# Kernel optimization log

Measured on AMD Instinct MI355X. Metric: run time of the kernel, lower is better.

The kernel has to match this reference:

```python
import jax, jax.numpy as jnp
import numpy as np
import math

B, N, L = 1, 256, 384
DM, DP, H, D = 256, 128, 8, 32  # d_msa, d_pair, n_head, d_hidden


def ln(x, g, b):
    m = x.mean(-1, keepdims=True)
    v = ((x - m) ** 2).mean(-1, keepdims=True)
    return (x - m) * jax.lax.rsqrt(v + 1e-5) * g + b


def setup_inputs() -> dict:
    key = jax.random.key(0)
    ks = jax.random.split(key, 12)
    s = 0.02
    return dict(
        msa=jax.random.normal(ks[0], (B, N, L, DM), jnp.float32),
        pair=jax.random.normal(ks[1], (B, L, L, DP), jnp.float32),
        ln_msa_g=jnp.ones((DM,), jnp.float32),
        ln_msa_b=jnp.zeros((DM,), jnp.float32),
        ln_pair_g=jnp.ones((DP,), jnp.float32),
        ln_pair_b=jnp.zeros((DP,), jnp.float32),
        sw_wq=s * jax.random.normal(ks[2], (DM, H * D), jnp.float32),
        sw_bq=jnp.zeros((H * D,), jnp.float32),
        sw_wk=s * jax.random.normal(ks[3], (DM, H * D), jnp.float32),
        sw_bk=jnp.zeros((H * D,), jnp.float32),
        wq=s * jax.random.normal(ks[4], (DM, H * D), jnp.float32),
        wk=s * jax.random.normal(ks[5], (DM, H * D), jnp.float32),
        wv=s * jax.random.normal(ks[6], (DM, H * D), jnp.float32),
        wb=s * jax.random.normal(ks[7], (DP, H), jnp.float32),
        wg=s * jax.random.normal(ks[8], (DM, H * D), jnp.float32),
        bg=jnp.ones((H * D,), jnp.float32),
        wo=s * jax.random.normal(ks[9], (H * D, DM), jnp.float32),
        bo=jnp.zeros((DM,), jnp.float32),
    )


def reference(msa, pair, ln_msa_g, ln_msa_b, ln_pair_g, ln_pair_b,
              sw_wq, sw_bq, sw_wk, sw_bk, wq, wk, wv, wb, wg, bg, wo, bo):
    m = ln(msa, ln_msa_g, ln_msa_b)  # (B,N,L,DM) -- LayerNorm(msa)
    inv_sqrt_d = 1.0 / math.sqrt(D)

    # --- SequenceWeight: attention of target seq (row 0) over all MSA rows ---
    qsw = ((m[:, 0] @ sw_wq) + sw_bq).reshape(B, 1, L, H, D) * inv_sqrt_d
    ksw = ((m @ sw_wk) + sw_bk).reshape(B, N, L, H, D)
    sw_logits = jnp.einsum('bqihd,bnihd->bnihq', qsw, ksw)  # (B,N,L,H,1)
    seq_weight = jax.nn.softmax(sw_logits, axis=1)  # softmax over MSA depth N; dropout is eval no-op

    # --- row attention with pair bias ---
    q = (m @ wq).reshape(B, N, L, H, D) * seq_weight  # query scaled by per-row seq weight
    k = (m @ wk).reshape(B, N, L, H, D) * inv_sqrt_d
    attn = jnp.einsum('bnihd,bnjhd->bijh', q, k)  # sum over MSA rows n -> (B,L,L,H)
    attn = attn + ln(pair, ln_pair_g, ln_pair_b) @ wb  # additive pair bias
    attn = jax.nn.softmax(attn, axis=-2)  # softmax over j (dim=-2)

    v = (m @ wv).reshape(B, N, L, H, D)
    out = jnp.einsum('bijh,bnjhd->bnihd', attn, v).reshape(B, N, L, H * D)
    gate = jax.nn.sigmoid((m @ wg) + bg)
    out = out * gate
    return out @ wo + bo  # (B,N,L,DM)
```

## Files before the change

kernel.cpp:

```cpp
#include <hip/hip_runtime.h>
#include <math.h>

typedef unsigned short u16;
typedef __bf16 bf16x8 __attribute__((ext_vector_type(8)));
typedef float f32x4 __attribute__((ext_vector_type(4)));

#define DEV static __device__ __forceinline__

DEV float b2f(u16 u) { union { unsigned int i; float f; } v; v.i = ((unsigned int)u) << 16; return v.f; }
DEV u16 f2b(float f) {
  union { float f; unsigned int i; } v; v.f = f;
  unsigned int x = v.i;
  unsigned int r = (x + 0x7fffu + ((x >> 16) & 1u)) >> 16;
  return (u16)r;
}
DEV bf16x8 load8bf(const u16* p) {
  union { uint4 u; bf16x8 b; } t;
  t.u = *(const uint4*)p;
  return t.b;
}
DEV float wave_sum(float x) {
  for (int m = 32; m >= 1; m >>= 1) x += __shfl_xor(x, m, 64);
  return x;
}
DEV float wave_max(float x) {
  for (int m = 32; m >= 1; m >>= 1) x = fmaxf(x, __shfl_xor(x, m, 64));
  return x;
}

__global__ __launch_bounds__(256) void detect_dtype(const u16* __restrict__ probe, int* __restrict__ flag) {
  __shared__ float red[4];
  int wave = threadIdx.x >> 6, lane = threadIdx.x & 63;
  float v = fabsf(b2f(probe[threadIdx.x]));
  v = wave_max(v);
  if (lane == 0) red[wave] = v;
  __syncthreads();
  if (threadIdx.x == 0) {
    float m = fmaxf(fmaxf(red[0], red[1]), fmaxf(red[2], red[3]));
    *flag = (m > 1e10f) ? 1 : 0;
  }
}

struct SmallCvt {
  const void* src[9];
  int n[9];
  int off[9];
};
__global__ __launch_bounds__(256) void cvt_small(SmallCvt s, u16* __restrict__ dst, const int* __restrict__ flagp) {
  int isf32 = *flagp;
  int a = blockIdx.x;
  const void* sp = s.src[a];
  for (int i = threadIdx.x; i < s.n[a]; i += 256) {
    float v = isf32 ? ((const float*)sp)[i] : b2f(((const u16*)sp)[i]);
    dst[s.off[a] + i] = f2b(v);
  }
}

__global__ __launch_bounds__(256) void ln_msa_k(const void* __restrict__ xv, const u16* __restrict__ g,
                                                const u16* __restrict__ b, u16* __restrict__ out,
                                                const int* __restrict__ flagp) {
  int isf32 = *flagp;
  int wave = threadIdx.x >> 6, lane = threadIdx.x & 63;
  size_t row = (size_t)blockIdx.x * 4 + wave;
  float f0, f1, f2, f3;
  if (isf32) {
    float4 v = *(const float4*)((const float*)xv + row * 256 + lane * 4);
    f0 = v.x; f1 = v.y; f2 = v.z; f3 = v.w;
  } else {
    ushort4 v = *(const ushort4*)((const u16*)xv + row * 256 + lane * 4);
    f0 = b2f(v.x); f1 = b2f(v.y); f2 = b2f(v.z); f3 = b2f(v.w);
  }
  float s = wave_sum(f0 + f1 + f2 + f3);
  float s2 = wave_sum(f0 * f0 + f1 * f1 + f2 * f2 + f3 * f3);
  float mean = s * (1.f / 256.f);
  float inv = rsqrtf(s2 * (1.f / 256.f) - mean * mean + 1e-5f);
  int c0 = lane * 4;
  ushort4 gv = *(const ushort4*)(g + c0);
  ushort4 bv = *(const ushort4*)(b + c0);
  ushort4 o;
  o.x = f2b((f0 - mean) * inv * b2f(gv.x) + b2f(bv.x));
  o.y = f2b((f1 - mean) * inv * b2f(gv.y) + b2f(bv.y));
  o.z = f2b((f2 - mean) * inv * b2f(gv.z) + b2f(bv.z));
  o.w = f2b((f3 - mean) * inv * b2f(gv.w) + b2f(bv.w));
  *(ushort4*)(out + row * 256 + c0) = o;
}

struct TransArgs {
  const void* src[7];
  u16* dst[7];
};
__global__ __launch_bounds__(256) void transpose_w(TransArgs t, const int* __restrict__ flagp) {
  __shared__ float tile[32][33];
  int isf32 = *flagp;
  int m = blockIdx.z;
  const void* s = t.src[m];
  u16* d = t.dst[m];
  int bx = blockIdx.x * 32, by = blockIdx.y * 32;
  int c = threadIdx.x & 31, r0 = threadIdx.x >> 5;
  for (int rr = r0; rr < 32; rr += 8) {
    int idx = (by + rr) * 256 + bx + c;
    tile[rr][c] = isf32 ? ((const float*)s)[idx] : b2f(((const u16*)s)[idx]);
  }
  __syncthreads();
  for (int rr = r0; rr < 32; rr += 8) d[(bx + rr) * 256 + by + c] = f2b(tile[c][rr]);
}

__global__ __launch_bounds__(256) void gemmA(const u16* __restrict__ A, size_t aoff,
                                             const u16* __restrict__ WT, const u16* __restrict__ bias,
                                             void* __restrict__ outv, size_t ooff, int mode, float alpha,
                                             const float* __restrict__ sw, int n0sw,
                                             const int* __restrict__ flagp, int out_flag,
                                             const u16* __restrict__ WT2, void* __restrict__ out2,
                                             int mode_b, float alpha_b) {
  int isf32 = *flagp;
  int n0;
  if (WT2) {
    if (blockIdx.y >> 1) { WT = WT2; outv = out2; mode = mode_b; alpha = alpha_b; bias = nullptr; }
    n0 = (blockIdx.y & 1) * 128;
  } else {
    n0 = blockIdx.y * 128;
  }
  int i0 = blockIdx.x * 128;
  int wave = threadIdx.x >> 6, lane = threadIdx.x & 63;
  int wr = wave >> 1, wc = wave & 1;
  int l15 = lane & 15, quad = lane >> 4;
  const f32x4 fz = {0.f, 0.f, 0.f, 0.f};
  f32x4 acc[4][4];
  for (int mi = 0; mi < 4; ++mi)
    for (int ni = 0; ni < 4; ++ni) acc[mi][ni] = fz;
  int arow = i0 + wr * 64 + l15;
  int brow = n0 + wc * 64 + l15;
  const u16* ap = A + (aoff + (size_t)arow) * 256 + quad * 8;
  const u16* bp = WT + (size_t)brow * 256 + quad * 8;
  for (int k0 = 0; k0 < 256; k0 += 32) {
    bf16x8 a[4], b[4];
#pragma unroll
    for (int mi = 0; mi < 4; ++mi) a[mi] = load8bf(ap + mi * 16 * 256 + k0);
#pragma unroll
    for (int ni = 0; ni < 4; ++ni) b[ni] = load8bf(bp + ni * 16 * 256 + k0);
#pragma unroll
    for (int mi = 0; mi < 4; ++mi)
#pragma unroll
      for (int ni = 0; ni < 4; ++ni)
        acc[mi][ni] = __builtin_amdgcn_mfma_f32_16x16x32_bf16(a[mi], b[ni], acc[mi][ni], 0, 0, 0);
  }
  int f32out = out_flag && isf32;
  int nloc = blockIdx.x / 3;
  if (mode == 3) {
#pragma unroll
    for (int mi = 0; mi < 4; ++mi) {
      int ib = i0 + wr * 64 + mi * 16 + quad * 4 - nloc * 384;
#pragma unroll
      for (int ni = 0; ni < 4; ++ni) {
        int col = n0 + wc * 64 + ni * 16 + l15;
        ushort4 o;
        o.x = f2b(acc[mi][ni][0]);
        o.y = f2b(acc[mi][ni][1]);
        o.z = f2b(acc[mi][ni][2]);
        o.w = f2b(acc[mi][ni][3]);
        *(ushort4*)((u16*)outv + ((size_t)(nloc * 256 + col)) * 384 + ib) = o;
      }
    }
    return;
  }
#pragma unroll
  for (int mi = 0; mi < 4; ++mi) {
    int rbase = i0 + wr * 64 + mi * 16 + quad * 4;
#pragma unroll
    for (int ni = 0; ni < 4; ++ni) {
      int col = n0 + wc * 64 + ni * 16 + l15;
      float bv = bias ? b2f(bias[col]) : 0.f;
#pragma unroll
      for (int r = 0; r < 4; ++r) {
        float val = (acc[mi][ni][r] + bv) * alpha;
        if (mode == 2) {
          int i = rbase - nloc * 384 + r;
          int h = col >> 5;
          val *= sw[((size_t)(i * 8 + h)) * 256 + (n0sw + nloc)];
        }
        size_t idx = (ooff + (size_t)(rbase + r)) * 256 + col;
        if (mode == 1) {
          float gate = 1.f / (1.f + expf(-val));
          ((u16*)outv)[idx] = f2b(b2f(((u16*)outv)[idx]) * gate);
        } else if (f32out) {
          ((float*)outv)[idx] = val;
        } else {
          ((u16*)outv)[idx] = f2b(val);
        }
      }
    }
  }
}

__global__ __launch_bounds__(256) void sw_logits_c(const u16* __restrict__ qsw, const u16* __restrict__ kswc,
                                                   float* __restrict__ swlog, int n0) {
  int nl = blockIdx.y;
  int t = blockIdx.x * 256 + threadIdx.x;
  int i = t >> 3, h = t & 7;
  const u16* kr = kswc + ((size_t)(nl * 384 + i)) * 256 + h * 32;
  const u16* qr = qsw + (size_t)i * 256 + h * 32;
  float dot = 0.f;
#pragma unroll
  for (int d8 = 0; d8 < 4; ++d8) {
    union { uint4 u; u16 us[8]; } ku, qu;
    ku.u = *(const uint4*)(kr + d8 * 8);
    qu.u = *(const uint4*)(qr + d8 * 8);
#pragma unroll
    for (int j = 0; j < 8; ++j) dot += b2f(ku.us[j]) * b2f(qu.us[j]);
  }
  swlog[(size_t)(i * 8 + h) * 256 + n0 + nl] = dot;
}

__global__ __launch_bounds__(256) void sw_softmax(float* __restrict__ swlog) {
  __shared__ float red[4];
  float* p = swlog + (size_t)blockIdx.x * 256;
  int wave = threadIdx.x >> 6, lane = threadIdx.x & 63;
  float x = p[threadIdx.x];
  float m = wave_max(x);
  if (lane == 0) red[wave] = m;
  __syncthreads();
  float mx = fmaxf(fmaxf(red[0], red[1]), fmaxf(red[2], red[3]));
  __syncthreads();
  float e = expf(x - mx);
  float s = wave_sum(e);
  if (lane == 0) red[wave] = s;
  __syncthreads();
  float sum = red[0] + red[1] + red[2] + red[3];
  p[threadIdx.x] = e / sum;
}

__global__ __launch_bounds__(256) void pair_bias(const void* __restrict__ pairv, const u16* __restrict__ g,
                                                 const u16* __restrict__ b, const u16* __restrict__ wb,
                                                 float* __restrict__ attn, const int* __restrict__ flagp) {
  int isf32 = *flagp;
  int wave = threadIdx.x >> 6, lane = threadIdx.x & 63;
  size_t row = (size_t)blockIdx.x * 4 + wave;
  float v0, v1;
  if (isf32) {
    const float* pf = (const float*)pairv + row * 128 + lane * 2;
    v0 = pf[0]; v1 = pf[1];
  } else {
    const u16* pr = (const u16*)pairv + row * 128 + lane * 2;
    v0 = b2f(pr[0]); v1 = b2f(pr[1]);
  }
  float s = wave_sum(v0 + v1);
  float s2 = wave_sum(v0 * v0 + v1 * v1);
  float mean = s * (1.f / 128.f);
  float var = s2 * (1.f / 128.f) - mean * mean;
  float inv = rsqrtf(var + 1e-5f);
  int c0 = lane * 2;
  v0 = (v0 - mean) * inv * b2f(g[c0]) + b2f(b[c0]);
  v1 = (v1 - mean) * inv * b2f(g[c0 + 1]) + b2f(b[c0 + 1]);
  float ph[8];
  const u16* w0 = wb + c0 * 8;
#pragma unroll
  for (int h = 0; h < 8; ++h) ph[h] = v0 * b2f(w0[h]) + v1 * b2f(w0[8 + h]);
#pragma unroll
  for (int m = 32; m >= 1; m >>= 1)
#pragma unroll
    for (int h = 0; h < 8; ++h) ph[h] += __shfl_xor(ph[h], m, 64);
  if (lane == 0) {
#pragma unroll
    for (int h = 0; h < 8; ++h) attn[(size_t)h * 147456 + row] = ph[h];
  }
}

__global__ __launch_bounds__(256) void qk_accum_c(const u16* __restrict__ qc, const u16* __restrict__ kc,
                                                  float* __restrict__ attn, int nlen) {
  int h = blockIdx.y;
  int i0 = (blockIdx.x % 3) * 128, j0 = (blockIdx.x / 3) * 128;
  int nb = blockIdx.z * nlen;
  int wave = threadIdx.x >> 6, lane = threadIdx.x & 63;
  int wr = wave >> 1, wc = wave & 1;
  int l15 = lane & 15, quad = lane >> 4;
  const f32x4 fz = {0.f, 0.f, 0.f, 0.f};
  f32x4 acc[4][4];
  for (int mi = 0; mi < 4; ++mi)
    for (int ni = 0; ni < 4; ++ni) acc[mi][ni] = fz;
  int arow = i0 + wr * 64 + l15;
  int brow = j0 + wc * 64 + l15;
  for (int n = nb; n < nb + nlen; ++n) {
    size_t base = (size_t)n * 384;
    const u16* ap = qc + (base + arow) * 256 + h * 32 + quad * 8;
    const u16* bp = kc + (base + brow) * 256 + h * 32 + quad * 8;
    bf16x8 a[4], b[4];
#pragma unroll
    for (int mi = 0; mi < 4; ++mi) a[mi] = load8bf(ap + mi * 16 * 256);
#pragma unroll
    for (int ni = 0; ni < 4; ++ni) b[ni] = load8bf(bp + ni * 16 * 256);
#pragma unroll
    for (int mi = 0; mi < 4; ++mi)
#pragma unroll
      for (int ni = 0; ni < 4; ++ni)
        acc[mi][ni] = __builtin_amdgcn_mfma_f32_16x16x32_bf16(a[mi], b[ni], acc[mi][ni], 0, 0, 0);
  }
#pragma unroll
  for (int mi = 0; mi < 4; ++mi)
#pragma unroll
    for (int ni = 0; ni < 4; ++ni) {
      int i = i0 + wr * 64 + mi * 16 + quad * 4;
      int j = j0 + wc * 64 + ni * 16 + l15;
#pragma unroll
      for (int r = 0; r < 4; ++r)
        atomicAdd(&attn[(size_t)h * 147456 + (size_t)(i + r) * 384 + j], acc[mi][ni][r]);
    }
}

__global__ __launch_bounds__(384) void attn_softmax_k(const float* __restrict__ attn, u16* __restrict__ attn_bf) {
  __shared__ float red[6];
  size_t r = blockIdx.x;
  const float* p = attn + r * 384;
  int wave = threadIdx.x >> 6, lane = threadIdx.x & 63;
  float x = p[threadIdx.x];
  float m = wave_max(x);
  if (lane == 0) red[wave] = m;
  __syncthreads();
  float mx = red[0];
#pragma unroll
  for (int i = 1; i < 6; ++i) mx = fmaxf(mx, red[i]);
  __syncthreads();
  float e = expf(x - mx);
  float s = wave_sum(e);
  if (lane == 0) red[wave] = s;
  __syncthreads();
  float sum = 0.f;
#pragma unroll
  for (int i = 0; i < 6; ++i) sum += red[i];
  attn_bf[r * 384 + threadIdx.x] = f2b(e / sum);
}

__global__ __launch_bounds__(256) void pv_gemm(const u16* __restrict__ attn_bf, const u16* __restrict__ vt,
                                               u16* __restrict__ oc) {
  int h = blockIdx.z;
  int i0 = blockIdx.x * 128;
  int c0 = blockIdx.y * 128;
  int wave = threadIdx.x >> 6, lane = threadIdx.x & 63;
  int wr = wave >> 1, wc = wave & 1;
  int l15 = lane & 15, quad = lane >> 4;
  const f32x4 fz = {0.f, 0.f, 0.f, 0.f};
  f32x4 acc[4][4];
  for (int mi = 0; mi < 4; ++mi)
    for (int ni = 0; ni < 4; ++ni) acc[mi][ni] = fz;
  int arow = i0 + wr * 64 + l15;
  const u16* ap = attn_bf + ((size_t)(h * 384 + arow)) * 384 + quad * 8;
  const u16* bp[4];
#pragma unroll
  for (int ni = 0; ni < 4; ++ni) {
    int col = c0 + wc * 64 + ni * 16 + l15;
    bp[ni] = vt + ((size_t)((col >> 5) * 256 + h * 32 + (col & 31))) * 384 + quad * 8;
  }
  for (int k0 = 0; k0 < 384; k0 += 32) {
    bf16x8 a[4], b[4];
#pragma unroll
    for (int mi = 0; mi < 4; ++mi) a[mi] = load8bf(ap + mi * 16 * 384 + k0);
#pragma unroll
    for (int ni = 0; ni < 4; ++ni) b[ni] = load8bf(bp[ni] + k0);
#pragma unroll
    for (int mi = 0; mi < 4; ++mi)
#pragma unroll
      for (int ni = 0; ni < 4; ++ni)
        acc[mi][ni] = __builtin_amdgcn_mfma_f32_16x16x32_bf16(a[mi], b[ni], acc[mi][ni], 0, 0, 0);
  }
#pragma unroll
  for (int mi = 0; mi < 4; ++mi) {
    int ib = i0 + wr * 64 + mi * 16 + quad * 4;
#pragma unroll
    for (int ni = 0; ni < 4; ++ni) {
      int col = c0 + wc * 64 + ni * 16 + l15;
      int nl = col >> 5, d = col & 31;
#pragma unroll
      for (int r = 0; r < 4; ++r)
        oc[((size_t)(nl * 384 + ib + r)) * 256 + h * 32 + d] = f2b(acc[mi][ni][r]);
    }
  }
}

extern "C" void kernel_launch(void* const* d_in, const int* in_sizes, int n_in,
                              void* d_out, int out_size, void* d_ws, size_t ws_size,
                              hipStream_t stream) {
  const void* msa = d_in[0];
  const void* pair = d_in[1];
  const void* ln_msa_g = d_in[2];
  const void* ln_msa_b = d_in[3];
  const void* ln_pair_g = d_in[4];
  const void* ln_pair_b = d_in[5];
  const void* sw_wq = d_in[6];
  const void* sw_bq = d_in[7];
  const void* sw_wk = d_in[8];
  const void* sw_bk = d_in[9];
  const void* wq = d_in[10];
  const void* wk = d_in[11];
  const void* wv = d_in[12];
  const void* wb = d_in[13];
  const void* wg = d_in[14];
  const void* bg = d_in[15];
  const void* wo = d_in[16];
  const void* bo = d_in[17];

  char* ws = (char*)d_ws;
  int* flag = (int*)ws;
  float* swlog = (float*)(ws + 256);
  float* attnf = (float*)(ws + 3145984);
  u16* wT = (u16*)(ws + 7864576);
  u16* qswb = (u16*)(ws + 8782080);
  u16* attnbf = (u16*)(ws + 8978688);
  u16* smallv = (u16*)(ws + 11337984);
  u16* mbf = (u16*)(ws + 11343616);
  const size_t SMALLS = 61675264ull;
  u16* c_lng = smallv + 0;
  u16* c_lnb = smallv + 256;
  u16* c_lpg = smallv + 512;
  u16* c_lpb = smallv + 640;
  u16* c_sbq = smallv + 768;
  u16* c_sbk = smallv + 1024;
  u16* c_bg = smallv + 1280;
  u16* c_bo = smallv + 1536;
  u16* c_wb = smallv + 1792;

  int NC = 256;
  while (NC > 8 && SMALLS + 3ull * (size_t)NC * 196608ull > ws_size) NC >>= 1;
  const size_t CBsz = (size_t)NC * 196608ull;
  u16* CB1 = (u16*)(ws + SMALLS);
  u16* CB2 = (u16*)(ws + SMALLS + CBsz);
  u16* CB3 = (u16*)(ws + SMALLS + 2 * CBsz);
  const int nchunks = 256 / NC;
  const int nlen = 8;

  const float isd = 0.17677669529663687f;

  detect_dtype<<<1, 256, 0, stream>>>((const u16*)msa, flag);

  SmallCvt sc;
  sc.src[0] = ln_msa_g;  sc.n[0] = 256;  sc.off[0] = 0;
  sc.src[1] = ln_msa_b;  sc.n[1] = 256;  sc.off[1] = 256;
  sc.src[2] = ln_pair_g; sc.n[2] = 128;  sc.off[2] = 512;
  sc.src[3] = ln_pair_b; sc.n[3] = 128;  sc.off[3] = 640;
  sc.src[4] = sw_bq;     sc.n[4] = 256;  sc.off[4] = 768;
  sc.src[5] = sw_bk;     sc.n[5] = 256;  sc.off[5] = 1024;
  sc.src[6] = bg;        sc.n[6] = 256;  sc.off[6] = 1280;
  sc.src[7] = bo;        sc.n[7] = 256;  sc.off[7] = 1536;
  sc.src[8] = wb;        sc.n[8] = 1024; sc.off[8] = 1792;
  cvt_small<<<9, 256, 0, stream>>>(sc, smallv, flag);

  TransArgs ta;
  ta.src[0] = sw_wq; ta.src[1] = sw_wk; ta.src[2] = wq; ta.src[3] = wk;
  ta.src[4] = wv;    ta.src[5] = wg;    ta.src[6] = wo;
  for (int i = 0; i < 7; ++i) ta.dst[i] = wT + i * 65536;
  transpose_w<<<dim3(8, 8, 7), 256, 0, stream>>>(ta, flag);

  ln_msa_k<<<24576, 256, 0, stream>>>(msa, c_lng, c_lnb, mbf, flag);

  gemmA<<<dim3(3, 2), 256, 0, stream>>>(mbf, 0, wT + 0 * 65536, c_sbq,
                                        qswb, 0, 0, isd, nullptr, 0, flag, 0,
                                        nullptr, nullptr, 0, 0.f);

  for (int c = 0; c < nchunks; ++c) {
    size_t R = (size_t)c * NC * 384;
    gemmA<<<dim3(3 * NC, 2), 256, 0, stream>>>(mbf, R, wT + 1 * 65536, c_sbk,
                                               CB1, 0, 0, 1.f, nullptr, 0, flag, 0,
                                               nullptr, nullptr, 0, 0.f);
    sw_logits_c<<<dim3(12, NC), 256, 0, stream>>>(qswb, CB1, swlog, c * NC);
  }
  sw_softmax<<<3072, 256, 0, stream>>>(swlog);

  pair_bias<<<36864, 256, 0, stream>>>(pair, c_lpg, c_lpb, c_wb, attnf, flag);
  for (int c = 0; c < nchunks; ++c) {
    size_t R = (size_t)c * NC * 384;
    gemmA<<<dim3(3 * NC, 4), 256, 0, stream>>>(mbf, R, wT + 2 * 65536, nullptr,
                                               CB1, 0, 2, 1.f, swlog, c * NC, flag, 0,
                                               wT + 3 * 65536, CB2, 0, isd);
    qk_accum_c<<<dim3(9, 8, NC / nlen), 256, 0, stream>>>(CB1, CB2, attnf, nlen);
  }
  attn_softmax_k<<<3072, 384, 0, stream>>>(attnf, attnbf);

  for (int c = 0; c < nchunks; ++c) {
    size_t R = (size_t)c * NC * 384;
    gemmA<<<dim3(3 * NC, 2), 256, 0, stream>>>(mbf, R, wT + 4 * 65536, nullptr,
                                               CB2, 0, 3, 1.f, nullptr, 0, flag, 0,
                                               nullptr, nullptr, 0, 0.f);
    pv_gemm<<<dim3(3, NC / 4, 8), 256, 0, stream>>>(attnbf, CB2, CB3);
    gemmA<<<dim3(3 * NC, 2), 256, 0, stream>>>(mbf, R, wT + 5 * 65536, c_bg,
                                               CB3, 0, 1, 1.f, nullptr, 0, flag, 0,
                                               nullptr, nullptr, 0, 0.f);
    gemmA<<<dim3(3 * NC, 2), 256, 0, stream>>>(CB3, 0, wT + 6 * 65536, c_bo,
                                               d_out, R, 0, 1.f, nullptr, 0, flag, 1,
                                               nullptr, nullptr, 0, 0.f);
  }
}
```

Baseline: 1.031 ms.

## Stage gemmA tiles through swizzled LDS via direct global-to-LDS loads

The projection GEMM used to load A and weight fragments straight from global memory into registers, with each wave reading its own rows. It now loads 128x64 tiles of A and W into shared memory using global_load_lds, with an XOR swizzle to avoid bank conflicts, and reads MFMA fragments from LDS so the block shares data between waves. A separate change raises nlen from 8 to 32 (capped at NC), altering a chunk length used elsewhere. The tile loads are not double-buffered, so each k-step pays a full sync and load latency.

```diff
diff --git a/kernel.cpp b/kernel.cpp
--- a/kernel.cpp
+++ b/kernel.cpp
@@ -18,6 +18,10 @@
   union { uint4 u; bf16x8 b; } t;
   t.u = *(const uint4*)p;
   return t.b;
+}
+DEV void gl_lds16(const u16* g, u16* l) {
+  __builtin_amdgcn_global_load_lds((const __attribute__((address_space(1))) unsigned int*)g,
+                                   (__attribute__((address_space(3))) unsigned int*)l, 16, 0, 0);
 }
 DEV float wave_sum(float x) {
   for (int m = 32; m >= 1; m >>= 1) x += __shfl_xor(x, m, 64);
@@ -112,6 +116,8 @@
                                              const int* __restrict__ flagp, int out_flag,
                                              const u16* __restrict__ WT2, void* __restrict__ out2,
                                              int mode_b, float alpha_b) {
+  __shared__ u16 As[128 * 64];
+  __shared__ u16 Bs[128 * 64];
   int isf32 = *flagp;
   int n0;
   if (WT2) {
@@ -121,28 +127,48 @@
     n0 = blockIdx.y * 128;
   }
   int i0 = blockIdx.x * 128;
-  int wave = threadIdx.x >> 6, lane = threadIdx.x & 63;
+  int t = threadIdx.x;
+  int wave = t >> 6, lane = t & 63;
   int wr = wave >> 1, wc = wave & 1;
   int l15 = lane & 15, quad = lane >> 4;
   const f32x4 fz = {0.f, 0.f, 0.f, 0.f};
   f32x4 acc[4][4];
   for (int mi = 0; mi < 4; ++mi)
     for (int ni = 0; ni < 4; ++ni) acc[mi][ni] = fz;
-  int arow = i0 + wr * 64 + l15;
-  int brow = n0 + wc * 64 + l15;
-  const u16* ap = A + (aoff + (size_t)arow) * 256 + quad * 8;
-  const u16* bp = WT + (size_t)brow * 256 + quad * 8;
-  for (int k0 = 0; k0 < 256; k0 += 32) {
-    bf16x8 a[4], b[4];
-#pragma unroll
-    for (int mi = 0; mi < 4; ++mi) a[mi] = load8bf(ap + mi * 16 * 256 + k0);
-#pragma unroll
-    for (int ni = 0; ni < 4; ++ni) b[ni] = load8bf(bp + ni * 16 * 256 + k0);
-#pragma unroll
-    for (int mi = 0; mi < 4; ++mi)
-#pragma unroll
-      for (int ni = 0; ni < 4; ++ni)
-        acc[mi][ni] = __builtin_amdgcn_mfma_f32_16x16x32_bf16(a[mi], b[ni], acc[mi][ni], 0, 0, 0);
+  int srow = t >> 3;
+  int scol = ((t & 7) ^ (srow & 7)) * 8;
+  const u16* ga = A + (aoff + (size_t)(i0 + srow)) * 256 + scol;
+  const u16* gb = WT + ((size_t)(n0 + srow)) * 256 + scol;
+  u16* la = As + t * 8;
+  u16* lb = Bs + t * 8;
+  for (int k0 = 0; k0 < 256; k0 += 64) {
+    __syncthreads();
+#pragma unroll
+    for (int p = 0; p < 4; ++p) {
+      gl_lds16(ga + (size_t)p * 32 * 256 + k0, la + p * 2048);
+      gl_lds16(gb + (size_t)p * 32 * 256 + k0, lb + p * 2048);
+    }
+    __syncthreads();
+#pragma unroll
+    for (int kk = 0; kk < 2; ++kk) {
+      bf16x8 a[4], b[4];
+      int kc = kk * 32 + quad * 8;
+#pragma unroll
+      for (int mi = 0; mi < 4; ++mi) {
+        int row = wr * 64 + mi * 16 + l15;
+        a[mi] = load8bf(As + row * 64 + (kc ^ ((row & 7) << 3)));
+      }
+#pragma unroll
+      for (int ni = 0; ni < 4; ++ni) {
+        int row = wc * 64 + ni * 16 + l15;
+        b[ni] = load8bf(Bs + row * 64 + (kc ^ ((row & 7) << 3)));
+      }
+#pragma unroll
+      for (int mi = 0; mi < 4; ++mi)
+#pragma unroll
+        for (int ni = 0; ni < 4; ++ni)
+          acc[mi][ni] = __builtin_amdgcn_mfma_f32_16x16x32_bf16(a[mi], b[ni], acc[mi][ni], 0, 0, 0);
+    }
   }
   int f32out = out_flag && isf32;
   int nloc = blockIdx.x / 3;
@@ -424,7 +450,7 @@
   u16* CB2 = (u16*)(ws + SMALLS + CBsz);
   u16* CB3 = (u16*)(ws + SMALLS + 2 * CBsz);
   const int nchunks = 256 / NC;
-  const int nlen = 8;
+  const int nlen = (NC < 32) ? NC : 32;
 
   const float isd = 0.17677669529663687f;
 
```

Result: faster. 865.7 us (-16.0%).
